# Kernel optimization log

Measured on AMD Instinct MI355X. Metric: run time of the kernel, lower is better.

Reference implementation:

```python
import jax, jax.numpy as jnp
import numpy as np

HIDDEN = 4096
N_HEADS = 32
N_KV_HEADS = 8
HEAD_DIM = HIDDEN // N_HEADS
KV_GROUPS = N_HEADS // N_KV_HEADS
TEMPERATURE = 1.0
NEG_INF = -1e9


def _bitlinear(x, W):
    """BitNet b1.58 BitLinear: per-token int8 activation quant + ternary weight quant (quant-dequant)."""
    # activation: absmax int8 per last dim
    a_scale = 127.0 / jnp.clip(jnp.max(jnp.abs(x), axis=-1, keepdims=True), 1e-5, None)
    xq = jnp.clip(jnp.round(x * a_scale), -128.0, 127.0) / a_scale
    # weight: ternary with mean-abs scale
    w_scale = jnp.clip(jnp.mean(jnp.abs(W)), 1e-5, None)
    Wq = jnp.clip(jnp.round(W / w_scale), -1.0, 1.0) * w_scale
    return jnp.einsum('bsh,oh->bso', xq, Wq)


def _base2_softmax(x, temperature=TEMPERATURE):
    # numerically stable 2^x softmax: 2^((x-m)/T) / sum
    m = jnp.max(x, axis=-1, keepdims=True)
    p = jnp.exp2((x - m) / temperature)
    return p / jnp.sum(p, axis=-1, keepdims=True)


def setup_inputs() -> dict:
    key = jax.random.key(0)
    ks = jax.random.split(key, 6)
    B, S = 2, 2048
    hidden_states = jax.random.normal(ks[0], (B, S, HIDDEN), dtype=jnp.float32)
    # additive causal mask [B, 1, S, S]
    causal = jnp.tril(jnp.ones((S, S), dtype=bool))
    attention_mask = jnp.where(causal, 0.0, NEG_INF).astype(jnp.float32)[None, None]
    attention_mask = jnp.broadcast_to(attention_mask, (B, 1, S, S))
    Wq = jax.random.normal(ks[1], (HIDDEN, HIDDEN), dtype=jnp.float32) * 0.02
    Wk = jax.random.normal(ks[2], (N_KV_HEADS * HEAD_DIM, HIDDEN), dtype=jnp.float32) * 0.02
    Wv = jax.random.normal(ks[3], (N_KV_HEADS * HEAD_DIM, HIDDEN), dtype=jnp.float32) * 0.02
    Wo = jax.random.normal(ks[4], (HIDDEN, HIDDEN), dtype=jnp.float32) * 0.02
    return {"hidden_states": hidden_states, "attention_mask": attention_mask,
            "Wq": Wq, "Wk": Wk, "Wv": Wv, "Wo": Wo}


def reference(hidden_states, attention_mask, Wq, Wk, Wv, Wo):
    B, S, _ = hidden_states.shape
    q = _bitlinear(hidden_states, Wq).reshape(B, S, N_HEADS, HEAD_DIM).transpose(0, 2, 1, 3)
    k = _bitlinear(hidden_states, Wk).reshape(B, S, N_KV_HEADS, HEAD_DIM).transpose(0, 2, 1, 3)
    v = _bitlinear(hidden_states, Wv).reshape(B, S, N_KV_HEADS, HEAD_DIM).transpose(0, 2, 1, 3)
    # GQA: repeat each kv head KV_GROUPS times along head dim
    k = jnp.repeat(k, KV_GROUPS, axis=1)
    v = jnp.repeat(v, KV_GROUPS, axis=1)
    attn_weights = jnp.einsum('bhqd,bhkd->bhqk', q, k) / np.sqrt(HEAD_DIM).astype(np.float32)
    attn_weights = attn_weights + attention_mask
    attn_weights = _base2_softmax(attn_weights)
    attn_output = jnp.einsum('bhqk,bhkd->bhqd', attn_weights, v)
    attn_output = attn_output.transpose(0, 2, 1, 3).reshape(B, S, HIDDEN)
    return _bitlinear(attn_output, Wo)
```

## Files before the change

kernel.cpp:

```cpp
#include <hip/hip_runtime.h>
#include <stdint.h>


typedef float  f32x4 __attribute__((ext_vector_type(4)));
typedef short  s16x8 __attribute__((ext_vector_type(8)));
typedef int    i32x4 __attribute__((ext_vector_type(4)));

__device__ __forceinline__ uint16_t f2b(float f) {
  uint32_t u = __float_as_uint(f);
  return (uint16_t)((u + 0x7FFFu + ((u >> 16) & 1u)) >> 16);
}
__device__ __forceinline__ uint32_t cvt_pk_bf16(float lo, float hi) {
  uint32_t r;
  asm("v_cvt_pk_bf16_f32 %0, %1, %2" : "=v"(r) : "v"(lo), "v"(hi));
  return r;
}
__device__ __forceinline__ void gl_lds16(const void* g, void* l) {
  __builtin_amdgcn_global_load_lds((const __attribute__((address_space(1))) unsigned int*)g,
                                   (__attribute__((address_space(3))) unsigned int*)l, 16, 0, 0);
}
__device__ __forceinline__ f32x4 mfma_bf16(s16x8 a, s16x8 b, f32x4 c) {
  return __builtin_amdgcn_mfma_f32_16x16x32_bf16(a, b, c, 0, 0, 0);
}
__device__ __forceinline__ i32x4 mfma_i8(i32x4 a, i32x4 b, i32x4 c) {
  return __builtin_amdgcn_mfma_i32_16x16x64_i8(a, b, c, 0, 0, 0);
}

__global__ __launch_bounds__(256) void k_qact_f32(const float* __restrict__ x,
                                                  int8_t* __restrict__ xq, float* __restrict__ rs) {
  __shared__ float red[4];
  const int row = blockIdx.x, t = threadIdx.x;
  const float4* xr = (const float4*)(x + (size_t)row * 4096);
  float v[16];
  #pragma unroll
  for (int i = 0; i < 4; i++) {
    float4 f = xr[t + 256 * i];
    v[i*4+0] = f.x; v[i*4+1] = f.y; v[i*4+2] = f.z; v[i*4+3] = f.w;
  }
  float mx = 0.f;
  #pragma unroll
  for (int i = 0; i < 16; i++) mx = fmaxf(mx, fabsf(v[i]));
  for (int o = 1; o < 64; o <<= 1) mx = fmaxf(mx, __shfl_xor(mx, o));
  if ((t & 63) == 0) red[t >> 6] = mx;
  __syncthreads();
  mx = fmaxf(fmaxf(red[0], red[1]), fmaxf(red[2], red[3]));
  mx = fmaxf(mx, 1e-5f);
  const float a = 127.f / mx;
  if (t == 0) rs[row] = mx * (1.f / 127.f);
  uint32_t* dst = (uint32_t*)(xq + (size_t)row * 4096);
  #pragma unroll
  for (int i = 0; i < 4; i++) {
    uint32_t w = 0;
    #pragma unroll
    for (int j = 0; j < 4; j++) {
      float q = rintf(v[i*4+j] * a);
      q = fmaxf(-128.f, fminf(127.f, q));
      w |= ((uint32_t)((int)q & 255)) << (j * 8);
    }
    dst[t + 256 * i] = w;
  }
}

__global__ __launch_bounds__(256) void k_abssum_part(const float* __restrict__ wq, const float* __restrict__ wk,
                                                     const float* __restrict__ wv, const float* __restrict__ wo,
                                                     double* __restrict__ part) {
  __shared__ double red[4];
  const int blk = blockIdx.x, t = threadIdx.x;
  const float* src; size_t base;
  if (blk < 1024)      { src = wq; base = (size_t)blk * 16384; }
  else if (blk < 1280) { src = wk; base = (size_t)(blk - 1024) * 16384; }
  else if (blk < 1536) { src = wv; base = (size_t)(blk - 1280) * 16384; }
  else                 { src = wo; base = (size_t)(blk - 1536) * 16384; }
  double s = 0.0;
  #pragma unroll
  for (int r = 0; r < 16; r++) {
    float4 f = *(const float4*)(src + base + r * 1024 + t * 4);
    s += (double)fabsf(f.x) + (double)fabsf(f.y) + (double)fabsf(f.z) + (double)fabsf(f.w);
  }
  for (int o = 1; o < 64; o <<= 1) s += __shfl_xor(s, o);
  if ((t & 63) == 0) red[t >> 6] = s;
  __syncthreads();
  if (t == 0) part[blk] = red[0] + red[1] + red[2] + red[3];
}

__global__ __launch_bounds__(256) void k_reduce_sums(const double* __restrict__ part, double* __restrict__ sums) {
  const int w = threadIdx.x >> 6, lane = threadIdx.x & 63;
  const int s0 = (w == 0) ? 0 : (w == 1) ? 1024 : (w == 2) ? 1280 : 1536;
  const int s1 = (w == 0) ? 1024 : (w == 1) ? 1280 : (w == 2) ? 1536 : 2560;
  double s = 0.0;
  for (int i = s0 + lane; i < s1; i += 64) s += part[i];
  for (int o = 1; o < 64; o <<= 1) s += __shfl_xor(s, o);
  if (lane == 0) sums[w] = s;
}

__global__ __launch_bounds__(256) void k_quant_w_all(const float* __restrict__ wq, const float* __restrict__ wk,
                                                     const float* __restrict__ wv, const float* __restrict__ wo,
                                                     int8_t* __restrict__ wqkv, int8_t* __restrict__ woq,
                                                     const double* __restrict__ sums) {
  const int blk = blockIdx.x, t = threadIdx.x;
  const float* src; int8_t* dst; size_t base; int sidx; double ivn;
  if (blk < 1024)      { src = wq; dst = wqkv;                        base = (size_t)blk * 16384;          sidx = 0; ivn = 1.0 / 16777216.0; }
  else if (blk < 1280) { src = wk; dst = wqkv + (size_t)4096 * 4096;  base = (size_t)(blk - 1024) * 16384; sidx = 1; ivn = 1.0 / 4194304.0;  }
  else if (blk < 1536) { src = wv; dst = wqkv + (size_t)5120 * 4096;  base = (size_t)(blk - 1280) * 16384; sidx = 2; ivn = 1.0 / 4194304.0;  }
  else                 { src = wo; dst = woq;                         base = (size_t)(blk - 1536) * 16384; sidx = 3; ivn = 1.0 / 16777216.0; }
  const float ws = (float)fmax(sums[sidx] * ivn, 1e-5);
  #pragma unroll
  for (int r = 0; r < 16; r++) {
    size_t e = base + r * 1024 + t * 4;
    float4 f = *(const float4*)(src + e);
    float hv[4] = {f.x, f.y, f.z, f.w};
    uint32_t w = 0;
    #pragma unroll
    for (int j = 0; j < 4; j++) {
      float q = rintf(hv[j] / ws);
      q = fmaxf(-1.f, fminf(1.f, q));
      w |= ((uint32_t)((int)q & 255)) << (j * 8);
    }
    *(uint32_t*)(dst + e) = w;
  }
}

template<int MODE>
__global__ __launch_bounds__(256) void k_gemm_i8(const int8_t* __restrict__ A, const int8_t* __restrict__ Bw,
                                                 const float* __restrict__ rs, const double* __restrict__ sums,
                                                 uint16_t* __restrict__ qb, uint16_t* __restrict__ kb,
                                                 uint16_t* __restrict__ vb, float* __restrict__ outp) {
  __shared__ int8_t lA[16384];
  __shared__ int8_t lB[16384];
  const int bn = blockIdx.x, bm = blockIdx.y;
  const int t = threadIdx.x, wave = t >> 6, lane = t & 63;
  const int quad = lane >> 4, l15 = lane & 15;
  const int wm = wave >> 1, wn = wave & 1;

  i32x4 acc[4][4];
  #pragma unroll
  for (int i = 0; i < 4; i++)
    #pragma unroll
    for (int j = 0; j < 4; j++) acc[i][j] = (i32x4){0, 0, 0, 0};

  const size_t arow0 = (size_t)bm * 128;
  const size_t brow0 = (size_t)bn * 128;

  for (int k0 = 0; k0 < 4096; k0 += 128) {
    #pragma unroll
    for (int r = 0; r < 4; r++) {
      int off = r * 4096 + wave * 1024 + lane * 16;
      int row = off >> 7;
      int pos = (off >> 4) & 7;
      int chunk = pos ^ (row & 7);
      gl_lds16(A  + (arow0 + row) * 4096 + k0 + chunk * 16, lA + r * 4096 + wave * 1024);
      gl_lds16(Bw + (brow0 + row) * 4096 + k0 + chunk * 16, lB + r * 4096 + wave * 1024);
    }
    __syncthreads();
    #pragma unroll
    for (int ks = 0; ks < 2; ks++) {
      i32x4 af[4], bf[4];
      #pragma unroll
      for (int i = 0; i < 4; i++) {
        int m = wm * 64 + i * 16 + l15;
        int c = ks * 4 + quad;
        af[i] = *(const i32x4*)(lA + m * 128 + (c ^ (m & 7)) * 16);
        int n = wn * 64 + i * 16 + l15;
        bf[i] = *(const i32x4*)(lB + n * 128 + (c ^ (n & 7)) * 16);
      }
      #pragma unroll
      for (int i = 0; i < 4; i++)
        #pragma unroll
        for (int j = 0; j < 4; j++)
          acc[i][j] = mfma_i8(af[i], bf[j], acc[i][j]);
    }
    __syncthreads();
  }

  float wsc; int sel = 0;
  if (MODE == 0) {
    if (bn < 32)      { wsc = (float)fmax(sums[0] * (1.0 / 16777216.0), 1e-5); sel = 0; }
    else if (bn < 40) { wsc = (float)fmax(sums[1] * (1.0 / 4194304.0),  1e-5); sel = 1; }
    else              { wsc = (float)fmax(sums[2] * (1.0 / 4194304.0),  1e-5); sel = 2; }
  } else {
    wsc = (float)fmax(sums[3] * (1.0 / 16777216.0), 1e-5);
  }
  #pragma unroll
  for (int i = 0; i < 4; i++) {
    #pragma unroll
    for (int r = 0; r < 4; r++) {
      int token = bm * 128 + wm * 64 + i * 16 + quad * 4 + r;
      float rv = rs[token] * wsc;
      #pragma unroll
      for (int j = 0; j < 4; j++) {
        int o = bn * 128 + wn * 64 + j * 16 + l15;
        float val = (float)acc[i][j][r] * rv;
        if (MODE == 0) {
          int b = token >> 11, s2 = token & 2047;
          if (sel == 0) {
            int hh = o >> 7, d = o & 127;
            qb[(((size_t)b * 32 + hh) * 2048 + s2) * 128 + d] = f2b(val * 0.08838834764831845f);
          } else if (sel == 1) {
            int o2 = o - 4096; int g = o2 >> 7, d = o2 & 127;
            kb[(((size_t)b * 8 + g) * 2048 + s2) * 128 + d] = f2b(val);
          } else {
            int o2 = o - 5120; int g = o2 >> 7, d = o2 & 127;
            vb[(((size_t)b * 8 + g) * 2048 + s2) * 128 + d] = f2b(val);
          }
        } else {
          outp[(size_t)token * 4096 + o] = val;
        }
      }
    }
  }
}

__global__ __launch_bounds__(256) void k_transpose_v(const uint16_t* __restrict__ v, uint16_t* __restrict__ vt) {
  __shared__ uint16_t tile[64][72];
  const int bs = blockIdx.x * 64, bd = blockIdx.y * 64, g = blockIdx.z;
  const int t = threadIdx.x;
  const uint16_t* src = v + ((size_t)g * 2048 + bs) * 128 + bd;
  #pragma unroll
  for (int it = 0; it < 2; it++) {
    int r = (t >> 3) + it * 32;
    int c = (t & 7) * 8;
    uint4 u = *(const uint4*)(src + (size_t)r * 128 + c);
    uint16_t* p = &tile[r][c];
    p[0] = u.x & 0xffff; p[1] = u.x >> 16; p[2] = u.y & 0xffff; p[3] = u.y >> 16;
    p[4] = u.z & 0xffff; p[5] = u.z >> 16; p[6] = u.w & 0xffff; p[7] = u.w >> 16;
  }
  __syncthreads();
  uint16_t* dst = vt + ((size_t)g * 128 + bd) * 2048 + bs;
  #pragma unroll
  for (int it = 0; it < 2; it++) {
    int r = (t >> 3) + it * 32;
    int c = (t & 7) * 8;
    uint32_t w0 = tile[c+0][r] | ((uint32_t)tile[c+1][r] << 16);
    uint32_t w1 = tile[c+2][r] | ((uint32_t)tile[c+3][r] << 16);
    uint32_t w2 = tile[c+4][r] | ((uint32_t)tile[c+5][r] << 16);
    uint32_t w3 = tile[c+6][r] | ((uint32_t)tile[c+7][r] << 16);
    *(uint4*)(dst + (size_t)r * 2048 + c) = make_uint4(w0, w1, w2, w3);
  }
}

__global__ __launch_bounds__(256, 4) void k_attn(const uint16_t* __restrict__ qg, const uint16_t* __restrict__ kg,
                                                 const uint16_t* __restrict__ vtg, float* __restrict__ attn) {
  __shared__ char smem[32768];
  const int p = blockIdx.x, bh = blockIdx.y;
  const int b = bh >> 5, h = bh & 31, kv = h >> 2;
  const int t = threadIdx.x, wave = t >> 6, lane = t & 63;
  const int quad = lane >> 4, l15 = lane & 15;

  const char* qbase = (const char*)(qg + (((size_t)b * 32 + h) * 2048) * 128);
  const char* ksrc  = (const char*)(kg + (((size_t)b * 8 + kv) * 2048) * 128);
  const char* vsrc  = (const char*)(vtg + (((size_t)b * 8 + kv) * 128) * 2048);

  for (int pass = 0; pass < 2; pass++) {
    const int qt = pass ? (31 - p) : p;

    __syncthreads();
    #pragma unroll
    for (int r = 0; r < 4; r++) {
      int off = r * 4096 + t * 16;
      int row = off >> 8, pos = (off >> 4) & 15;
      int chunk = pos ^ (row & 7);
      gl_lds16(qbase + (size_t)(qt * 64 + row) * 256 + chunk * 16, smem + off);
    }
    __syncthreads();
    s16x8 qf[4];
    #pragma unroll
    for (int ks = 0; ks < 4; ks++) {
      int n = wave * 16 + l15;
      int c = ks * 4 + quad;
      qf[ks] = *(const s16x8*)(smem + n * 256 + ((c ^ (n & 7))) * 16);
    }

    float Mx = -3.0e38f, Ls = 0.f;
    f32x4 Ov[8];
    #pragma unroll
    for (int mf = 0; mf < 8; mf++) Ov[mf] = (f32x4){0, 0, 0, 0};

    for (int kt = 0; kt <= qt; kt++) {
      __syncthreads();
      #pragma unroll
      for (int r = 0; r < 4; r++) {
        int off = r * 4096 + t * 16;
        { int row = off >> 8, pos = (off >> 4) & 15, chunk = pos ^ (row & 7);
          gl_lds16(ksrc + (size_t)(kt * 64 + row) * 256 + chunk * 16, smem + off); }
        { int row = off >> 7, pos = (off >> 4) & 7, chunk = pos ^ (row & 7);
          gl_lds16(vsrc + (size_t)row * 4096 + kt * 128 + chunk * 16, smem + 16384 + off); }
      }
      __syncthreads();

      f32x4 sc[4];
      #pragma unroll
      for (int mf = 0; mf < 4; mf++) sc[mf] = (f32x4){0, 0, 0, 0};
      __builtin_amdgcn_s_setprio(1);
      #pragma unroll
      for (int ks = 0; ks < 4; ks++) {
        #pragma unroll
        for (int mf = 0; mf < 4; mf++) {
          int m = mf * 16 + l15;
          int c = ks * 4 + quad;
          s16x8 kf = *(const s16x8*)(smem + m * 256 + ((c ^ (m & 7))) * 16);
          sc[mf] = mfma_bf16(kf, qf[ks], sc[mf]);
        }
      }
      __builtin_amdgcn_s_setprio(0);

      if (kt == qt) {
        int qloc = wave * 16 + l15;
        #pragma unroll
        for (int mf = 0; mf < 4; mf++)
          #pragma unroll
          for (int r = 0; r < 4; r++) {
            int kloc = mf * 16 + quad * 4 + r;
            if (kloc > qloc) sc[mf][r] = -3.0e38f;
          }
      }

      float x = sc[0][0];
      #pragma unroll
      for (int mf = 0; mf < 4; mf++)
        #pragma unroll
        for (int r = 0; r < 4; r++) x = fmaxf(x, sc[mf][r]);
      x = fmaxf(x, __shfl_xor(x, 16));
      x = fmaxf(x, __shfl_xor(x, 32));
      if (!__all(x - Mx <= 8.f)) {
        float m2 = fmaxf(Mx, x);
        float al = exp2f(Mx - m2);
        Mx = m2;
        Ls *= al;
        #pragma unroll
        for (int mf = 0; mf < 8; mf++)
          #pragma unroll
          for (int r = 0; r < 4; r++) Ov[mf][r] *= al;
      }
      float s = 0.f;
      #pragma unroll
      for (int mf = 0; mf < 4; mf++)
        #pragma unroll
        for (int r = 0; r < 4; r++) {
          float pv = exp2f(sc[mf][r] - Mx);
          sc[mf][r] = pv;
          s += pv;
        }
      s += __shfl_xor(s, 16);
      s += __shfl_xor(s, 32);
      Ls += s;

      #pragma unroll
      for (int ks = 0; ks < 2; ks++) {
        uint32_t pk[2][2];
        #pragma unroll
        for (int mfp = 0; mfp < 2; mfp++)
          #pragma unroll
          for (int pr = 0; pr < 2; pr++)
            pk[mfp][pr] = cvt_pk_bf16(sc[2*ks+mfp][2*pr], sc[2*ks+mfp][2*pr+1]);
        uint32_t pf[4];
        #pragma unroll
        for (int j2 = 0; j2 < 4; j2++) {
          int srcLane = ((quad & 1) * 2 + (j2 >> 1)) * 16 + l15;
          uint32_t a0 = __shfl(pk[0][j2 & 1], srcLane);
          uint32_t a1 = __shfl(pk[1][j2 & 1], srcLane);
          pf[j2] = (quad >= 2) ? a1 : a0;
        }
        s16x8 pfr = *(const s16x8*)&pf[0];
        __builtin_amdgcn_s_setprio(1);
        #pragma unroll
        for (int mf = 0; mf < 8; mf++) {
          int m = mf * 16 + l15;
          int c = ks * 4 + quad;
          s16x8 vf = *(const s16x8*)(smem + 16384 + m * 128 + ((c ^ (m & 7))) * 16);
          Ov[mf] = mfma_bf16(vf, pfr, Ov[mf]);
        }
        __builtin_amdgcn_s_setprio(0);
      }
    }

    float inv = 1.f / Ls;
    size_t token = (size_t)b * 2048 + qt * 64 + wave * 16 + l15;
    float* obase = attn + token * 4096 + h * 128 + quad * 4;
    #pragma unroll
    for (int mf = 0; mf < 8; mf++) {
      float4 v4 = make_float4(Ov[mf][0] * inv, Ov[mf][1] * inv, Ov[mf][2] * inv, Ov[mf][3] * inv);
      *(float4*)(obase + mf * 16) = v4;
    }
  }
}

extern "C" void kernel_launch(void* const* d_in, const int* in_sizes, int n_in,
                              void* d_out, int out_size, void* d_ws, size_t ws_size,
                              hipStream_t stream) {
  (void)in_sizes; (void)out_size;
  if (n_in < 6) return;
  const float* hs = (const float*)d_in[0];
  const float* Wq = (const float*)d_in[2];
  const float* Wk = (const float*)d_in[3];
  const float* Wv = (const float*)d_in[4];
  const float* Wo = (const float*)d_in[5];
  float* out = (float*)d_out;

  char* p = (char*)d_ws;
  size_t off = 0;
  auto take = [&](size_t bytes) { char* r = p + off; off += (bytes + 255) & ~(size_t)255; return r; };
  int8_t*   xq1  = (int8_t*)  take((size_t)4096 * 4096);
  float*    rs1  = (float*)   take(4096 * 4);
  int8_t*   wqkv = (int8_t*)  take((size_t)6144 * 4096);
  int8_t*   woq  = (int8_t*)  take((size_t)4096 * 4096);
  uint16_t* qb   = (uint16_t*)take((size_t)2 * 32 * 2048 * 128 * 2);
  uint16_t* kb   = (uint16_t*)take((size_t)2 * 8 * 2048 * 128 * 2);
  uint16_t* vb   = (uint16_t*)take((size_t)2 * 8 * 2048 * 128 * 2);
  uint16_t* vtb  = (uint16_t*)take((size_t)2 * 8 * 2048 * 128 * 2);
  float*    attn = (float*)   take((size_t)4096 * 4096 * 4);
  int8_t*   xq2  = (int8_t*)  take((size_t)4096 * 4096);
  float*    rs2  = (float*)   take(4096 * 4);
  double*   part = (double*)  take(2560 * 8);
  double*   sums = (double*)  take(256);
  if (off > ws_size) return;

  k_abssum_part<<<2560, 256, 0, stream>>>(Wq, Wk, Wv, Wo, part);
  k_reduce_sums<<<1, 256, 0, stream>>>(part, sums);
  k_quant_w_all<<<2560, 256, 0, stream>>>(Wq, Wk, Wv, Wo, wqkv, woq, sums);
  k_qact_f32<<<4096, 256, 0, stream>>>(hs, xq1, rs1);
  k_gemm_i8<0><<<dim3(48, 32), 256, 0, stream>>>(xq1, wqkv, rs1, sums, qb, kb, vb, (float*)nullptr);
  k_transpose_v<<<dim3(32, 2, 16), 256, 0, stream>>>(vb, vtb);
  k_attn<<<dim3(16, 64), 256, 0, stream>>>(qb, kb, vtb, attn);
  k_qact_f32<<<4096, 256, 0, stream>>>(attn, xq2, rs2);
  k_gemm_i8<1><<<dim3(32, 32), 256, 0, stream>>>(xq2, woq, rs2, sums,
                                                 (uint16_t*)nullptr, (uint16_t*)nullptr, (uint16_t*)nullptr, out);
}
```

Measured before the change: 667.9 us.

## Process 128-row query tiles per attention block to reuse K/V tiles

Each attention block now loads a 128-row query tile as two 64-row halves and computes both against every K/V tile it stages in shared memory. This halves global and LDS K/V traffic and barrier rounds per query row. It doubles the accumulator and score registers, lowers the occupancy hint to 2 blocks per CU, halves the grid, and computes one fully masked key tile on the diagonal.

```diff
diff --git a/kernel.cpp b/kernel.cpp
--- a/kernel.cpp
+++ b/kernel.cpp
@@ -238,7 +238,7 @@
   }
 }
 
-__global__ __launch_bounds__(256, 4) void k_attn(const uint16_t* __restrict__ qg, const uint16_t* __restrict__ kg,
+__global__ __launch_bounds__(256, 2) void k_attn(const uint16_t* __restrict__ qg, const uint16_t* __restrict__ kg,
                                                  const uint16_t* __restrict__ vtg, float* __restrict__ attn) {
   __shared__ char smem[32768];
   const int p = blockIdx.x, bh = blockIdx.y;
@@ -251,31 +251,37 @@
   const char* vsrc  = (const char*)(vtg + (((size_t)b * 8 + kv) * 128) * 2048);
 
   for (int pass = 0; pass < 2; pass++) {
-    const int qt = pass ? (31 - p) : p;
+    const int qt = pass ? (15 - p) : p;
 
     __syncthreads();
     #pragma unroll
-    for (int r = 0; r < 4; r++) {
+    for (int r = 0; r < 8; r++) {
       int off = r * 4096 + t * 16;
       int row = off >> 8, pos = (off >> 4) & 15;
       int chunk = pos ^ (row & 7);
-      gl_lds16(qbase + (size_t)(qt * 64 + row) * 256 + chunk * 16, smem + off);
+      gl_lds16(qbase + (size_t)(qt * 128 + row) * 256 + chunk * 16, smem + off);
     }
     __syncthreads();
-    s16x8 qf[4];
-    #pragma unroll
-    for (int ks = 0; ks < 4; ks++) {
-      int n = wave * 16 + l15;
-      int c = ks * 4 + quad;
-      qf[ks] = *(const s16x8*)(smem + n * 256 + ((c ^ (n & 7))) * 16);
-    }
-
-    float Mx = -3.0e38f, Ls = 0.f;
-    f32x4 Ov[8];
-    #pragma unroll
-    for (int mf = 0; mf < 8; mf++) Ov[mf] = (f32x4){0, 0, 0, 0};
-
-    for (int kt = 0; kt <= qt; kt++) {
+    s16x8 qf[2][4];
+    #pragma unroll
+    for (int hh = 0; hh < 2; hh++)
+      #pragma unroll
+      for (int ks = 0; ks < 4; ks++) {
+        int n = hh * 64 + wave * 16 + l15;
+        int c = ks * 4 + quad;
+        qf[hh][ks] = *(const s16x8*)(smem + n * 256 + ((c ^ (n & 7))) * 16);
+      }
+
+    float Mx[2] = {-3.0e38f, -3.0e38f};
+    float Ls[2] = {0.f, 0.f};
+    f32x4 Ov[2][8];
+    #pragma unroll
+    for (int hh = 0; hh < 2; hh++)
+      #pragma unroll
+      for (int mf = 0; mf < 8; mf++) Ov[hh][mf] = (f32x4){0, 0, 0, 0};
+
+    const int nkt = 2 * qt + 1;
+    for (int kt = 0; kt <= nkt; kt++) {
       __syncthreads();
       #pragma unroll
       for (int r = 0; r < 4; r++) {
@@ -287,9 +293,11 @@
       }
       __syncthreads();
 
-      f32x4 sc[4];
-      #pragma unroll
-      for (int mf = 0; mf < 4; mf++) sc[mf] = (f32x4){0, 0, 0, 0};
+      f32x4 sc[2][4];
+      #pragma unroll
+      for (int hh = 0; hh < 2; hh++)
+        #pragma unroll
+        for (int mf = 0; mf < 4; mf++) sc[hh][mf] = (f32x4){0, 0, 0, 0};
       __builtin_amdgcn_s_setprio(1);
       #pragma unroll
       for (int ks = 0; ks < 4; ks++) {
@@ -298,88 +306,105 @@
           int m = mf * 16 + l15;
           int c = ks * 4 + quad;
           s16x8 kf = *(const s16x8*)(smem + m * 256 + ((c ^ (m & 7))) * 16);
-          sc[mf] = mfma_bf16(kf, qf[ks], sc[mf]);
+          sc[0][mf] = mfma_bf16(kf, qf[0][ks], sc[0][mf]);
+          sc[1][mf] = mfma_bf16(kf, qf[1][ks], sc[1][mf]);
         }
       }
       __builtin_amdgcn_s_setprio(0);
 
-      if (kt == qt) {
-        int qloc = wave * 16 + l15;
+      #pragma unroll
+      for (int hh = 0; hh < 2; hh++) {
+        if (kt >= 2 * qt + hh) {
+          int qloc = hh * 64 + wave * 16 + l15;
+          int kb = (kt - 2 * qt) * 64;
+          #pragma unroll
+          for (int mf = 0; mf < 4; mf++)
+            #pragma unroll
+            for (int r = 0; r < 4; r++) {
+              int kloc = kb + mf * 16 + quad * 4 + r;
+              if (kloc > qloc) sc[hh][mf][r] = -3.0e38f;
+            }
+        }
+      }
+
+      #pragma unroll
+      for (int hh = 0; hh < 2; hh++) {
+        float x = sc[hh][0][0];
         #pragma unroll
         for (int mf = 0; mf < 4; mf++)
           #pragma unroll
+          for (int r = 0; r < 4; r++) x = fmaxf(x, sc[hh][mf][r]);
+        x = fmaxf(x, __shfl_xor(x, 16));
+        x = fmaxf(x, __shfl_xor(x, 32));
+        if (!__all(x - Mx[hh] <= 8.f)) {
+          float m2 = fmaxf(Mx[hh], x);
+          float al = exp2f(Mx[hh] - m2);
+          Mx[hh] = m2;
+          Ls[hh] *= al;
+          #pragma unroll
+          for (int mf = 0; mf < 8; mf++)
+            #pragma unroll
+            for (int r = 0; r < 4; r++) Ov[hh][mf][r] *= al;
+        }
+        float s = 0.f;
+        #pragma unroll
+        for (int mf = 0; mf < 4; mf++)
+          #pragma unroll
           for (int r = 0; r < 4; r++) {
-            int kloc = mf * 16 + quad * 4 + r;
-            if (kloc > qloc) sc[mf][r] = -3.0e38f;
+            float pv = exp2f(sc[hh][mf][r] - Mx[hh]);
+            sc[hh][mf][r] = pv;
+            s += pv;
           }
-      }
-
-      float x = sc[0][0];
-      #pragma unroll
-      for (int mf = 0; mf < 4; mf++)
-        #pragma unroll
-        for (int r = 0; r < 4; r++) x = fmaxf(x, sc[mf][r]);
-      x = fmaxf(x, __shfl_xor(x, 16));
-      x = fmaxf(x, __shfl_xor(x, 32));
-      if (!__all(x - Mx <= 8.f)) {
-        float m2 = fmaxf(Mx, x);
-        float al = exp2f(Mx - m2);
-        Mx = m2;
-        Ls *= al;
-        #pragma unroll
-        for (int mf = 0; mf < 8; mf++)
-          #pragma unroll
-          for (int r = 0; r < 4; r++) Ov[mf][r] *= al;
-      }
-      float s = 0.f;
-      #pragma unroll
-      for (int mf = 0; mf < 4; mf++)
-        #pragma unroll
-        for (int r = 0; r < 4; r++) {
-          float pv = exp2f(sc[mf][r] - Mx);
-          sc[mf][r] = pv;
-          s += pv;
-        }
-      s += __shfl_xor(s, 16);
-      s += __shfl_xor(s, 32);
-      Ls += s;
+        s += __shfl_xor(s, 16);
+        s += __shfl_xor(s, 32);
+        Ls[hh] += s;
+      }
 
       #pragma unroll
       for (int ks = 0; ks < 2; ks++) {
-        uint32_t pk[2][2];
-        #pragma unroll
-        for (int mfp = 0; mfp < 2; mfp++)
-          #pragma unroll
-          for (int pr = 0; pr < 2; pr++)
-            pk[mfp][pr] = cvt_pk_bf16(sc[2*ks+mfp][2*pr], sc[2*ks+mfp][2*pr+1]);
-        uint32_t pf[4];
-        #pragma unroll
-        for (int j2 = 0; j2 < 4; j2++) {
-          int srcLane = ((quad & 1) * 2 + (j2 >> 1)) * 16 + l15;
-          uint32_t a0 = __shfl(pk[0][j2 & 1], srcLane);
-          uint32_t a1 = __shfl(pk[1][j2 & 1], srcLane);
-          pf[j2] = (quad >= 2) ? a1 : a0;
-        }
-        s16x8 pfr = *(const s16x8*)&pf[0];
+        uint32_t pfw[2][4];
+        #pragma unroll
+        for (int hh = 0; hh < 2; hh++) {
+          uint32_t pk[2][2];
+          #pragma unroll
+          for (int mfp = 0; mfp < 2; mfp++)
+            #pragma unroll
+            for (int pr = 0; pr < 2; pr++)
+              pk[mfp][pr] = cvt_pk_bf16(sc[hh][2*ks+mfp][2*pr], sc[hh][2*ks+mfp][2*pr+1]);
+          #pragma unroll
+          for (int j2 = 0; j2 < 4; j2++) {
+            int srcLane = ((quad & 1) * 2 + (j2 >> 1)) * 16 + l15;
+            uint32_t a0 = __shfl(pk[0][j2 & 1], srcLane);
+            uint32_t a1 = __shfl(pk[1][j2 & 1], srcLane);
+            pfw[hh][j2] = (quad >= 2) ? a1 : a0;
+          }
+        }
+        s16x8 pfr0 = *(const s16x8*)&pfw[0][0];
+        s16x8 pfr1 = *(const s16x8*)&pfw[1][0];
         __builtin_amdgcn_s_setprio(1);
         #pragma unroll
         for (int mf = 0; mf < 8; mf++) {
           int m = mf * 16 + l15;
           int c = ks * 4 + quad;
           s16x8 vf = *(const s16x8*)(smem + 16384 + m * 128 + ((c ^ (m & 7))) * 16);
-          Ov[mf] = mfma_bf16(vf, pfr, Ov[mf]);
+          Ov[0][mf] = mfma_bf16(vf, pfr0, Ov[0][mf]);
+          Ov[1][mf] = mfma_bf16(vf, pfr1, Ov[1][mf]);
         }
         __builtin_amdgcn_s_setprio(0);
       }
     }
 
-    float inv = 1.f / Ls;
-    size_t token = (size_t)b * 2048 + qt * 64 + wave * 16 + l15;
-    float* obase = attn + token * 4096 + h * 128 + quad * 4;
-    #pragma unroll
-    for (int mf = 0; mf < 8; mf++) {
-      float4 v4 = make_float4(Ov[mf][0] * inv, Ov[mf][1] * inv, Ov[mf][2] * inv, Ov[mf][3] * inv);
-      *(float4*)(obase + mf * 16) = v4;
+    #pragma unroll
+    for (int hh = 0; hh < 2; hh++) {
+      float inv = 1.f / Ls[hh];
+      size_t token = (size_t)b * 2048 + qt * 128 + hh * 64 + wave * 16 + l15;
+      float* obase = attn + token * 4096 + h * 128 + quad * 4;
+      #pragma unroll
+      for (int mf = 0; mf < 8; mf++) {
+        float4 v4 = make_float4(Ov[hh][mf][0] * inv, Ov[hh][mf][1] * inv,
+                                Ov[hh][mf][2] * inv, Ov[hh][mf][3] * inv);
+        *(float4*)(obase + mf * 16) = v4;
+      }
     }
   }
 }
@@ -420,7 +445,7 @@
   k_qact_f32<<<4096, 256, 0, stream>>>(hs, xq1, rs1);
   k_gemm_i8<0><<<dim3(48, 32), 256, 0, stream>>>(xq1, wqkv, rs1, sums, qb, kb, vb, (float*)nullptr);
   k_transpose_v<<<dim3(32, 2, 16), 256, 0, stream>>>(vb, vtb);
-  k_attn<<<dim3(16, 64), 256, 0, stream>>>(qb, kb, vtb, attn);
+  k_attn<<<dim3(8, 64), 256, 0, stream>>>(qb, kb, vtb, attn);
   k_qact_f32<<<4096, 256, 0, stream>>>(attn, xq2, rs2);
   k_gemm_i8<1><<<dim3(32, 32), 256, 0, stream>>>(xq2, woq, rs2, sums,
                                                  (uint16_t*)nullptr, (uint16_t*)nullptr, (uint16_t*)nullptr, out);
```

New measurement: 655.9 us. About the same (-1.8%).
